# Kernel optimization log

Measured on AMD Instinct MI355X. Metric: run time of the kernel, lower is better.

Reference implementation:

```python
import jax, jax.numpy as jnp
import numpy as np

N_NODES = 20000
N_EDGES = 640000
IN_FEATS = 128
H1, H2 = 64, 32


def setup_inputs() -> dict:
    key = jax.random.key(0)
    ks = jax.random.split(key, 7)
    features = jax.random.normal(ks[0], (N_NODES, IN_FEATS), dtype=jnp.float32)
    W1 = jax.random.normal(ks[1], (IN_FEATS, H1), dtype=jnp.float32) * (1.0 / np.sqrt(IN_FEATS))
    b1 = jax.random.normal(ks[2], (H1,), dtype=jnp.float32) * 0.01
    W2 = jax.random.normal(ks[3], (H1, H2), dtype=jnp.float32) * (1.0 / np.sqrt(H1))
    b2 = jax.random.normal(ks[4], (H2,), dtype=jnp.float32) * 0.01
    src = jax.random.randint(ks[5], (N_EDGES,), 0, N_NODES, dtype=jnp.int32)
    dst = jax.random.randint(ks[6], (N_EDGES,), 0, N_NODES, dtype=jnp.int32)
    return {"features": features, "W1": W1, "b1": b1, "W2": W2, "b2": b2,
            "src": src, "dst": dst}


def _gcn_aggregate(h, src, dst, n_nodes):
    # copy_u + sum: gather source-node features along edges, sum at destinations
    return jax.ops.segment_sum(h[src], dst, num_segments=n_nodes)


def reference(features, W1, b1, W2, b2, src, dst):
    n = features.shape[0]
    # layer 1: aggregate then linear, relu
    h = _gcn_aggregate(features, src, dst, n)          # [N, in_feats]
    x = jax.nn.relu(h @ W1 + b1)                       # [N, 64]
    # layer 2: aggregate then linear
    h2 = _gcn_aggregate(x, src, dst, n)                # [N, 64]
    return h2 @ W2 + b2                                # [N, 32]
```

## Files before the change

kernel.cpp:

```cpp
#include <hip/hip_runtime.h>


#define NF 128
#define H1 64
#define H2 32
#define CAP 128
#define CAPSH 7
#define NG8 8

__device__ __forceinline__ float blo(unsigned u) { return __uint_as_float(u << 16); }
__device__ __forceinline__ float bhi(unsigned u) { return __uint_as_float(u & 0xffff0000u); }
__device__ __forceinline__ unsigned short f2b(float f) {
    unsigned x = __float_as_uint(f);
    return (unsigned short)((x + 0x7fffu + ((x >> 16) & 1u)) >> 16);
}

__global__ void zero_kernel(int* __restrict__ cnt, int n) {
    int i = blockIdx.x * blockDim.x + threadIdx.x;
    if (i < n) cnt[i] = 0;
}

__global__ void fill_kernel(const int* __restrict__ src, const int* __restrict__ dst,
                            int* __restrict__ cnt, unsigned short* __restrict__ slots,
                            int n_edges, int n_nodes) {
    int g = blockIdx.x & (NG8 - 1);
    int gi = blockIdx.x >> 3;
    int sz = (n_nodes + NG8 - 1) / NG8;
    int lo = g * sz;
    unsigned span = (unsigned)(min(lo + sz, n_nodes) - lo);
    int i4 = (gi * blockDim.x + threadIdx.x) * 4;
    if (i4 + 4 <= n_edges) {
        int4 d = *(const int4*)(dst + i4);
        int4 s = *(const int4*)(src + i4);
        int p;
        if ((unsigned)(d.x - lo) < span) { p = atomicAdd(&cnt[d.x], 1); if (p < CAP) slots[(d.x << CAPSH) + p] = (unsigned short)s.x; }
        if ((unsigned)(d.y - lo) < span) { p = atomicAdd(&cnt[d.y], 1); if (p < CAP) slots[(d.y << CAPSH) + p] = (unsigned short)s.y; }
        if ((unsigned)(d.z - lo) < span) { p = atomicAdd(&cnt[d.z], 1); if (p < CAP) slots[(d.z << CAPSH) + p] = (unsigned short)s.z; }
        if ((unsigned)(d.w - lo) < span) { p = atomicAdd(&cnt[d.w], 1); if (p < CAP) slots[(d.w << CAPSH) + p] = (unsigned short)s.w; }
    } else {
        for (int k = i4; k < n_edges; ++k) {
            int d = dst[k];
            if ((unsigned)(d - lo) < span) {
                int p = atomicAdd(&cnt[d], 1);
                if (p < CAP) slots[(d << CAPSH) + p] = (unsigned short)src[k];
            }
        }
    }
}

__launch_bounds__(256)
__global__ void gemm1_kernel(const float* __restrict__ F, const float* __restrict__ W1,
                             unsigned short* __restrict__ P1b, int n_nodes) {
    __shared__ float w[NF][H1];
    const float4* w4 = (const float4*)W1;
    float4* ws4 = (float4*)&w[0][0];
#pragma unroll
    for (int j = 0; j < 8; ++j) ws4[threadIdx.x + 256 * j] = w4[threadIdx.x + 256 * j];
    __syncthreads();
    int wid = threadIdx.x >> 6, lane = threadIdx.x & 63;
#pragma unroll
    for (int r = 0; r < 8; ++r) {
        int row = blockIdx.x * 32 + wid * 8 + r;
        if (row >= n_nodes) break;
        const float4* f4 = (const float4*)(F + (size_t)row * NF);
        float acc = 0.f;
#pragma unroll
        for (int k4 = 0; k4 < NF / 4; ++k4) {
            float4 fv = f4[k4];
            acc += fv.x * w[k4 * 4 + 0][lane];
            acc += fv.y * w[k4 * 4 + 1][lane];
            acc += fv.z * w[k4 * 4 + 2][lane];
            acc += fv.w * w[k4 * 4 + 3][lane];
        }
        P1b[(size_t)row * H1 + lane] = f2b(acc);
    }
}

__launch_bounds__(256)
__global__ void agg1gemm2_kernel(const unsigned short* __restrict__ P1b,
                                 const int* __restrict__ cnt, const unsigned short* __restrict__ slots,
                                 const float* __restrict__ b1, const float* __restrict__ W2,
                                 unsigned short* __restrict__ P2b, int n_nodes) {
    __shared__ float w[H1][H2];
    __shared__ float arow[4][H1];
    const float4* w4 = (const float4*)W2;
    float4* ws4 = (float4*)&w[0][0];
#pragma unroll
    for (int j = 0; j < 2; ++j) ws4[threadIdx.x + 256 * j] = w4[threadIdx.x + 256 * j];
    __syncthreads();
    int wid = threadIdx.x >> 6, lane = threadIdx.x & 63;
    int g = blockIdx.x & (NG8 - 1), gi = blockIdx.x >> 3;
    int sz = (n_nodes + NG8 - 1) / NG8;
    int ni = gi * 4 + wid;
    if (ni >= sz) return;
    int node = g * sz + ni;
    if (node >= n_nodes) return;
    int deg = min(cnt[node], CAP);
    int base = node << CAPSH;
    int half = lane >> 5, c = lane & 31;
    const unsigned* P1u = (const unsigned*)P1b;
    float ax = 0.f, ay = 0.f, bx = 0.f, by = 0.f;
    int i = 0;
    for (; i + 4 <= deg; i += 4) {
        int s0 = slots[base + i + half];
        int s1 = slots[base + i + 2 + half];
        unsigned u0 = P1u[(s0 << 5) + c];
        unsigned u1 = P1u[(s1 << 5) + c];
        ax += blo(u0); ay += bhi(u0);
        bx += blo(u1); by += bhi(u1);
    }
    for (; i + 2 <= deg; i += 2) {
        int s0 = slots[base + i + half];
        unsigned u0 = P1u[(s0 << 5) + c];
        ax += blo(u0); ay += bhi(u0);
    }
    if (i < deg && half == 0) {
        int s0 = slots[base + i];
        unsigned u0 = P1u[(s0 << 5) + c];
        ax += blo(u0); ay += bhi(u0);
    }
    ax += bx; ay += by;
    ax += __shfl_xor(ax, 32, 64);
    ay += __shfl_xor(ay, 32, 64);
    float2 bb = *(const float2*)(b1 + 2 * c);
    float v0 = fmaxf(ax + bb.x, 0.f), v1 = fmaxf(ay + bb.y, 0.f);
    if (lane < 32) *(float2*)&arow[wid][2 * c] = make_float2(v0, v1);
    int kb = half * 32;
    float acc2 = 0.f;
#pragma unroll
    for (int k = 0; k < 32; ++k) acc2 += arow[wid][kb + k] * w[kb + k][c];
    acc2 += __shfl_xor(acc2, 32, 64);
    if (lane < 32) P2b[(size_t)node * H2 + c] = f2b(acc2);
}

__launch_bounds__(256)
__global__ void agg2_kernel(const unsigned short* __restrict__ P2b,
                            const int* __restrict__ cnt, const unsigned short* __restrict__ slots,
                            const float* __restrict__ b2, float* __restrict__ out, int n_nodes) {
    int g = blockIdx.x & (NG8 - 1), gi = blockIdx.x >> 3;
    int sz = (n_nodes + NG8 - 1) / NG8;
    int ni = gi * 8 + (threadIdx.x >> 5);
    if (ni >= sz) return;
    int node = g * sz + ni;
    if (node >= n_nodes) return;
    int l = threadIdx.x & 31;
    int sub = l >> 4, c = l & 15;
    int deg = min(cnt[node], CAP);
    int base = node << CAPSH;
    const unsigned* P2u = (const unsigned*)P2b;
    float ax = 0.f, ay = 0.f, bx = 0.f, by = 0.f;
    int i = 0;
    for (; i + 4 <= deg; i += 4) {
        int s0 = slots[base + i + sub];
        int s1 = slots[base + i + 2 + sub];
        unsigned u0 = P2u[(s0 << 4) + c];
        unsigned u1 = P2u[(s1 << 4) + c];
        ax += blo(u0); ay += bhi(u0);
        bx += blo(u1); by += bhi(u1);
    }
    for (; i + 2 <= deg; i += 2) {
        int s0 = slots[base + i + sub];
        unsigned u0 = P2u[(s0 << 4) + c];
        ax += blo(u0); ay += bhi(u0);
    }
    if (i < deg && sub == 0) {
        int s0 = slots[base + i];
        unsigned u0 = P2u[(s0 << 4) + c];
        ax += blo(u0); ay += bhi(u0);
    }
    ax += bx; ay += by;
    ax += __shfl_xor(ax, 16, 64);
    ay += __shfl_xor(ay, 16, 64);
    if (sub == 0) {
        float2 bb = *(const float2*)(b2 + 2 * c);
        *(float2*)(out + (size_t)node * H2 + 2 * c) = make_float2(ax + bb.x, ay + bb.y);
    }
}

extern "C" void kernel_launch(void* const* d_in, const int* in_sizes, int n_in,
                              void* d_out, int out_size, void* d_ws, size_t ws_size,
                              hipStream_t stream) {
    const float* F  = (const float*)d_in[0];
    const float* W1 = (const float*)d_in[1];
    const float* b1 = (const float*)d_in[2];
    const float* W2 = (const float*)d_in[3];
    const float* b2 = (const float*)d_in[4];
    const int* src  = (const int*)d_in[5];
    const int* dst  = (const int*)d_in[6];
    float* out = (float*)d_out;

    int n_nodes = in_sizes[0] / NF;
    int n_edges = in_sizes[5];

    unsigned short* P1b = (unsigned short*)d_ws;
    unsigned short* P2b = P1b + (size_t)n_nodes * H1;
    unsigned short* slots = P2b + (size_t)n_nodes * H2;
    int* cnt = (int*)(slots + ((size_t)n_nodes << CAPSH));

    int sz = (n_nodes + NG8 - 1) / NG8;

    zero_kernel<<<(n_nodes + 255) / 256, 256, 0, stream>>>(cnt, n_nodes);

    int bpg_fill = ((n_edges + 3) / 4 + 255) / 256;
    fill_kernel<<<bpg_fill * NG8, 256, 0, stream>>>(src, dst, cnt, slots, n_edges, n_nodes);

    gemm1_kernel<<<(n_nodes + 31) / 32, 256, 0, stream>>>(F, W1, P1b, n_nodes);

    int bpg_a1 = (sz + 3) / 4;
    agg1gemm2_kernel<<<bpg_a1 * NG8, 256, 0, stream>>>(P1b, cnt, slots, b1, W2, P2b, n_nodes);

    int bpg_a2 = (sz + 7) / 8;
    agg2_kernel<<<bpg_a2 * NG8, 256, 0, stream>>>(P2b, cnt, slots, b2, out, n_nodes);
}
```

Baseline: 100.2 us.

## Bucket edges by destination group before slot fill and widen aggregation gathers

Replaces the 8x-replicated fill pass, where every block reread all edges and filtered by node group, with a staging kernel. The staging kernel bins packed (dst,src) pairs into per-group buffers using shared-memory counters and one global atomic per group. A second fill kernel then processes only its group's edges. Counter zeroing is folded into the first GEMM kernel, which removes a launch. Both aggregation kernels now gather 8-byte bf16 quads with more edges in flight per wavefront, adding extra shuffle reductions and a staging buffer with a fixed capacity margin.

```diff
diff --git a/kernel.cpp b/kernel.cpp
--- a/kernel.cpp
+++ b/kernel.cpp
@@ -7,6 +7,7 @@
 #define CAP 128
 #define CAPSH 7
 #define NG8 8
+#define FILL_BPG 80
 
 __device__ __forceinline__ float blo(unsigned u) { return __uint_as_float(u << 16); }
 __device__ __forceinline__ float bhi(unsigned u) { return __uint_as_float(u & 0xffff0000u); }
@@ -15,42 +16,12 @@
     return (unsigned short)((x + 0x7fffu + ((x >> 16) & 1u)) >> 16);
 }
 
-__global__ void zero_kernel(int* __restrict__ cnt, int n) {
-    int i = blockIdx.x * blockDim.x + threadIdx.x;
-    if (i < n) cnt[i] = 0;
-}
-
-__global__ void fill_kernel(const int* __restrict__ src, const int* __restrict__ dst,
-                            int* __restrict__ cnt, unsigned short* __restrict__ slots,
-                            int n_edges, int n_nodes) {
-    int g = blockIdx.x & (NG8 - 1);
-    int gi = blockIdx.x >> 3;
-    int sz = (n_nodes + NG8 - 1) / NG8;
-    int lo = g * sz;
-    unsigned span = (unsigned)(min(lo + sz, n_nodes) - lo);
-    int i4 = (gi * blockDim.x + threadIdx.x) * 4;
-    if (i4 + 4 <= n_edges) {
-        int4 d = *(const int4*)(dst + i4);
-        int4 s = *(const int4*)(src + i4);
-        int p;
-        if ((unsigned)(d.x - lo) < span) { p = atomicAdd(&cnt[d.x], 1); if (p < CAP) slots[(d.x << CAPSH) + p] = (unsigned short)s.x; }
-        if ((unsigned)(d.y - lo) < span) { p = atomicAdd(&cnt[d.y], 1); if (p < CAP) slots[(d.y << CAPSH) + p] = (unsigned short)s.y; }
-        if ((unsigned)(d.z - lo) < span) { p = atomicAdd(&cnt[d.z], 1); if (p < CAP) slots[(d.z << CAPSH) + p] = (unsigned short)s.z; }
-        if ((unsigned)(d.w - lo) < span) { p = atomicAdd(&cnt[d.w], 1); if (p < CAP) slots[(d.w << CAPSH) + p] = (unsigned short)s.w; }
-    } else {
-        for (int k = i4; k < n_edges; ++k) {
-            int d = dst[k];
-            if ((unsigned)(d - lo) < span) {
-                int p = atomicAdd(&cnt[d], 1);
-                if (p < CAP) slots[(d << CAPSH) + p] = (unsigned short)src[k];
-            }
-        }
-    }
-}
-
 __launch_bounds__(256)
 __global__ void gemm1_kernel(const float* __restrict__ F, const float* __restrict__ W1,
-                             unsigned short* __restrict__ P1b, int n_nodes) {
+                             unsigned short* __restrict__ P1b, int* __restrict__ cntz,
+                             int n_zero, int n_nodes) {
+    int idx = blockIdx.x * 256 + threadIdx.x;
+    if (idx < n_zero) cntz[idx] = 0;
     __shared__ float w[NF][H1];
     const float4* w4 = (const float4*)W1;
     float4* ws4 = (float4*)&w[0][0];
@@ -77,10 +48,81 @@
 }
 
 __launch_bounds__(256)
+__global__ void stage_kernel(const int* __restrict__ src, const int* __restrict__ dst,
+                             unsigned* __restrict__ staged, int* __restrict__ gcur,
+                             int n_edges, int sz, int capg) {
+    __shared__ int lcnt[NG8];
+    __shared__ int lbase[NG8];
+    int t = threadIdx.x;
+    if (t < NG8) lcnt[t] = 0;
+    __syncthreads();
+    int i4 = (blockIdx.x * 256 + t) * 4;
+    int dd[4], ss[4], bb[4], pp[4];
+    if (i4 + 4 <= n_edges) {
+        int4 d4 = *(const int4*)(dst + i4);
+        int4 s4 = *(const int4*)(src + i4);
+        dd[0] = d4.x; dd[1] = d4.y; dd[2] = d4.z; dd[3] = d4.w;
+        ss[0] = s4.x; ss[1] = s4.y; ss[2] = s4.z; ss[3] = s4.w;
+    } else {
+#pragma unroll
+        for (int k = 0; k < 4; ++k) {
+            int e = i4 + k;
+            dd[k] = (e < n_edges) ? dst[e] : -1;
+            ss[k] = (e < n_edges) ? src[e] : 0;
+        }
+    }
+#pragma unroll
+    for (int k = 0; k < 4; ++k) {
+        if (dd[k] >= 0) {
+            bb[k] = (unsigned)dd[k] / (unsigned)sz;
+            pp[k] = atomicAdd(&lcnt[bb[k]], 1);
+        }
+    }
+    __syncthreads();
+    if (t < NG8) lbase[t] = lcnt[t] ? atomicAdd(&gcur[t], lcnt[t]) : 0;
+    __syncthreads();
+#pragma unroll
+    for (int k = 0; k < 4; ++k) {
+        if (dd[k] >= 0) {
+            int pos = lbase[bb[k]] + pp[k];
+            if (pos < capg)
+                staged[(size_t)bb[k] * capg + pos] = ((unsigned)dd[k] << 16) | (unsigned)ss[k];
+        }
+    }
+}
+
+__launch_bounds__(256)
+__global__ void fill2_kernel(const unsigned* __restrict__ staged, const int* __restrict__ gcur,
+                             int* __restrict__ cnt, unsigned short* __restrict__ slots,
+                             int capg) {
+    int g = blockIdx.x & (NG8 - 1), gi = blockIdx.x >> 3;
+    int ecnt = min(gcur[g], capg);
+    const unsigned* sg = staged + (size_t)g * capg;
+    int stride = FILL_BPG * 256 * 4;
+    for (int j = (gi * 256 + threadIdx.x) * 4; j < ecnt; j += stride) {
+        if (j + 4 <= ecnt) {
+            uint4 u = *(const uint4*)(sg + j);
+            int d, p;
+            d = u.x >> 16; p = atomicAdd(&cnt[d], 1); if (p < CAP) slots[(d << CAPSH) + p] = (unsigned short)(u.x & 0xffffu);
+            d = u.y >> 16; p = atomicAdd(&cnt[d], 1); if (p < CAP) slots[(d << CAPSH) + p] = (unsigned short)(u.y & 0xffffu);
+            d = u.z >> 16; p = atomicAdd(&cnt[d], 1); if (p < CAP) slots[(d << CAPSH) + p] = (unsigned short)(u.z & 0xffffu);
+            d = u.w >> 16; p = atomicAdd(&cnt[d], 1); if (p < CAP) slots[(d << CAPSH) + p] = (unsigned short)(u.w & 0xffffu);
+        } else {
+            for (int k = j; k < ecnt; ++k) {
+                unsigned u = sg[k];
+                int d = u >> 16;
+                int p = atomicAdd(&cnt[d], 1);
+                if (p < CAP) slots[(d << CAPSH) + p] = (unsigned short)(u & 0xffffu);
+            }
+        }
+    }
+}
+
+__launch_bounds__(256)
 __global__ void agg1gemm2_kernel(const unsigned short* __restrict__ P1b,
                                  const int* __restrict__ cnt, const unsigned short* __restrict__ slots,
                                  const float* __restrict__ b1, const float* __restrict__ W2,
-                                 unsigned short* __restrict__ P2b, int n_nodes) {
+                                 unsigned short* __restrict__ P2b, int n_nodes, int sz) {
     __shared__ float w[H1][H2];
     __shared__ float arow[4][H1];
     const float4* w4 = (const float4*)W2;
@@ -90,90 +132,106 @@
     __syncthreads();
     int wid = threadIdx.x >> 6, lane = threadIdx.x & 63;
     int g = blockIdx.x & (NG8 - 1), gi = blockIdx.x >> 3;
-    int sz = (n_nodes + NG8 - 1) / NG8;
     int ni = gi * 4 + wid;
     if (ni >= sz) return;
     int node = g * sz + ni;
     if (node >= n_nodes) return;
     int deg = min(cnt[node], CAP);
     int base = node << CAPSH;
-    int half = lane >> 5, c = lane & 31;
-    const unsigned* P1u = (const unsigned*)P1b;
-    float ax = 0.f, ay = 0.f, bx = 0.f, by = 0.f;
+    int q = lane >> 4, c = lane & 15;
+    const uint2* P1v = (const uint2*)P1b;
+    float a0 = 0.f, a1 = 0.f, a2 = 0.f, a3 = 0.f;
+    float c0 = 0.f, c1 = 0.f, c2 = 0.f, c3 = 0.f;
     int i = 0;
+    for (; i + 8 <= deg; i += 8) {
+        int sA = slots[base + i + q];
+        int sB = slots[base + i + 4 + q];
+        uint2 uA = P1v[(sA << 4) + c];
+        uint2 uB = P1v[(sB << 4) + c];
+        a0 += blo(uA.x); a1 += bhi(uA.x); a2 += blo(uA.y); a3 += bhi(uA.y);
+        c0 += blo(uB.x); c1 += bhi(uB.x); c2 += blo(uB.y); c3 += bhi(uB.y);
+    }
     for (; i + 4 <= deg; i += 4) {
-        int s0 = slots[base + i + half];
-        int s1 = slots[base + i + 2 + half];
-        unsigned u0 = P1u[(s0 << 5) + c];
-        unsigned u1 = P1u[(s1 << 5) + c];
-        ax += blo(u0); ay += bhi(u0);
-        bx += blo(u1); by += bhi(u1);
-    }
-    for (; i + 2 <= deg; i += 2) {
-        int s0 = slots[base + i + half];
-        unsigned u0 = P1u[(s0 << 5) + c];
-        ax += blo(u0); ay += bhi(u0);
-    }
-    if (i < deg && half == 0) {
-        int s0 = slots[base + i];
-        unsigned u0 = P1u[(s0 << 5) + c];
-        ax += blo(u0); ay += bhi(u0);
-    }
-    ax += bx; ay += by;
-    ax += __shfl_xor(ax, 32, 64);
-    ay += __shfl_xor(ay, 32, 64);
-    float2 bb = *(const float2*)(b1 + 2 * c);
-    float v0 = fmaxf(ax + bb.x, 0.f), v1 = fmaxf(ay + bb.y, 0.f);
-    if (lane < 32) *(float2*)&arow[wid][2 * c] = make_float2(v0, v1);
+        int sA = slots[base + i + q];
+        uint2 uA = P1v[(sA << 4) + c];
+        a0 += blo(uA.x); a1 += bhi(uA.x); a2 += blo(uA.y); a3 += bhi(uA.y);
+    }
+    int r = deg - i;
+    if (q < r) {
+        int sA = slots[base + i + q];
+        uint2 uA = P1v[(sA << 4) + c];
+        a0 += blo(uA.x); a1 += bhi(uA.x); a2 += blo(uA.y); a3 += bhi(uA.y);
+    }
+    a0 += c0; a1 += c1; a2 += c2; a3 += c3;
+    a0 += __shfl_xor(a0, 16, 64); a0 += __shfl_xor(a0, 32, 64);
+    a1 += __shfl_xor(a1, 16, 64); a1 += __shfl_xor(a1, 32, 64);
+    a2 += __shfl_xor(a2, 16, 64); a2 += __shfl_xor(a2, 32, 64);
+    a3 += __shfl_xor(a3, 16, 64); a3 += __shfl_xor(a3, 32, 64);
+    if (q == 0) {
+        float4 bb = *(const float4*)(b1 + 4 * c);
+        float4 v;
+        v.x = fmaxf(a0 + bb.x, 0.f);
+        v.y = fmaxf(a1 + bb.y, 0.f);
+        v.z = fmaxf(a2 + bb.z, 0.f);
+        v.w = fmaxf(a3 + bb.w, 0.f);
+        *(float4*)&arow[wid][4 * c] = v;
+    }
+    int half = lane >> 5, c32 = lane & 31;
     int kb = half * 32;
     float acc2 = 0.f;
 #pragma unroll
-    for (int k = 0; k < 32; ++k) acc2 += arow[wid][kb + k] * w[kb + k][c];
+    for (int k = 0; k < 32; ++k) acc2 += arow[wid][kb + k] * w[kb + k][c32];
     acc2 += __shfl_xor(acc2, 32, 64);
-    if (lane < 32) P2b[(size_t)node * H2 + c] = f2b(acc2);
+    if (lane < 32) P2b[(size_t)node * H2 + c32] = f2b(acc2);
 }
 
 __launch_bounds__(256)
 __global__ void agg2_kernel(const unsigned short* __restrict__ P2b,
                             const int* __restrict__ cnt, const unsigned short* __restrict__ slots,
-                            const float* __restrict__ b2, float* __restrict__ out, int n_nodes) {
+                            const float* __restrict__ b2, float* __restrict__ out,
+                            int n_nodes, int sz) {
+    int wid = threadIdx.x >> 6, lane = threadIdx.x & 63;
     int g = blockIdx.x & (NG8 - 1), gi = blockIdx.x >> 3;
-    int sz = (n_nodes + NG8 - 1) / NG8;
-    int ni = gi * 8 + (threadIdx.x >> 5);
+    int ni = gi * 4 + wid;
     if (ni >= sz) return;
     int node = g * sz + ni;
     if (node >= n_nodes) return;
-    int l = threadIdx.x & 31;
-    int sub = l >> 4, c = l & 15;
     int deg = min(cnt[node], CAP);
     int base = node << CAPSH;
-    const unsigned* P2u = (const unsigned*)P2b;
-    float ax = 0.f, ay = 0.f, bx = 0.f, by = 0.f;
+    int o = lane >> 3, c = lane & 7;
+    const uint2* P2v = (const uint2*)P2b;
+    float a0 = 0.f, a1 = 0.f, a2 = 0.f, a3 = 0.f;
+    float c0 = 0.f, c1 = 0.f, c2 = 0.f, c3 = 0.f;
     int i = 0;
-    for (; i + 4 <= deg; i += 4) {
-        int s0 = slots[base + i + sub];
-        int s1 = slots[base + i + 2 + sub];
-        unsigned u0 = P2u[(s0 << 4) + c];
-        unsigned u1 = P2u[(s1 << 4) + c];
-        ax += blo(u0); ay += bhi(u0);
-        bx += blo(u1); by += bhi(u1);
-    }
-    for (; i + 2 <= deg; i += 2) {
-        int s0 = slots[base + i + sub];
-        unsigned u0 = P2u[(s0 << 4) + c];
-        ax += blo(u0); ay += bhi(u0);
-    }
-    if (i < deg && sub == 0) {
-        int s0 = slots[base + i];
-        unsigned u0 = P2u[(s0 << 4) + c];
-        ax += blo(u0); ay += bhi(u0);
-    }
-    ax += bx; ay += by;
-    ax += __shfl_xor(ax, 16, 64);
-    ay += __shfl_xor(ay, 16, 64);
-    if (sub == 0) {
-        float2 bb = *(const float2*)(b2 + 2 * c);
-        *(float2*)(out + (size_t)node * H2 + 2 * c) = make_float2(ax + bb.x, ay + bb.y);
+    for (; i + 16 <= deg; i += 16) {
+        int sA = slots[base + i + o];
+        int sB = slots[base + i + 8 + o];
+        uint2 uA = P2v[(sA << 3) + c];
+        uint2 uB = P2v[(sB << 3) + c];
+        a0 += blo(uA.x); a1 += bhi(uA.x); a2 += blo(uA.y); a3 += bhi(uA.y);
+        c0 += blo(uB.x); c1 += bhi(uB.x); c2 += blo(uB.y); c3 += bhi(uB.y);
+    }
+    for (; i + 8 <= deg; i += 8) {
+        int sA = slots[base + i + o];
+        uint2 uA = P2v[(sA << 3) + c];
+        a0 += blo(uA.x); a1 += bhi(uA.x); a2 += blo(uA.y); a3 += bhi(uA.y);
+    }
+    int r = deg - i;
+    if (o < r) {
+        int sA = slots[base + i + o];
+        uint2 uA = P2v[(sA << 3) + c];
+        a0 += blo(uA.x); a1 += bhi(uA.x); a2 += blo(uA.y); a3 += bhi(uA.y);
+    }
+    a0 += c0; a1 += c1; a2 += c2; a3 += c3;
+    a0 += __shfl_xor(a0, 8, 64); a0 += __shfl_xor(a0, 16, 64); a0 += __shfl_xor(a0, 32, 64);
+    a1 += __shfl_xor(a1, 8, 64); a1 += __shfl_xor(a1, 16, 64); a1 += __shfl_xor(a1, 32, 64);
+    a2 += __shfl_xor(a2, 8, 64); a2 += __shfl_xor(a2, 16, 64); a2 += __shfl_xor(a2, 32, 64);
+    a3 += __shfl_xor(a3, 8, 64); a3 += __shfl_xor(a3, 16, 64); a3 += __shfl_xor(a3, 32, 64);
+    if (o == 0) {
+        float4 bb = *(const float4*)(b2 + 4 * c);
+        float4 v;
+        v.x = a0 + bb.x; v.y = a1 + bb.y; v.z = a2 + bb.z; v.w = a3 + bb.w;
+        *(float4*)(out + (size_t)node * H2 + 4 * c) = v;
     }
 }
 
@@ -191,24 +249,23 @@
 
     int n_nodes = in_sizes[0] / NF;
     int n_edges = in_sizes[5];
+    int sz = (n_nodes + NG8 - 1) / NG8;
+    int capg = n_edges / NG8 + 8192;
 
     unsigned short* P1b = (unsigned short*)d_ws;
     unsigned short* P2b = P1b + (size_t)n_nodes * H1;
     unsigned short* slots = P2b + (size_t)n_nodes * H2;
     int* cnt = (int*)(slots + ((size_t)n_nodes << CAPSH));
-
-    int sz = (n_nodes + NG8 - 1) / NG8;
-
-    zero_kernel<<<(n_nodes + 255) / 256, 256, 0, stream>>>(cnt, n_nodes);
-
-    int bpg_fill = ((n_edges + 3) / 4 + 255) / 256;
-    fill_kernel<<<bpg_fill * NG8, 256, 0, stream>>>(src, dst, cnt, slots, n_edges, n_nodes);
-
-    gemm1_kernel<<<(n_nodes + 31) / 32, 256, 0, stream>>>(F, W1, P1b, n_nodes);
-
-    int bpg_a1 = (sz + 3) / 4;
-    agg1gemm2_kernel<<<bpg_a1 * NG8, 256, 0, stream>>>(P1b, cnt, slots, b1, W2, P2b, n_nodes);
-
-    int bpg_a2 = (sz + 7) / 8;
-    agg2_kernel<<<bpg_a2 * NG8, 256, 0, stream>>>(P2b, cnt, slots, b2, out, n_nodes);
-}
+    int* gcur = cnt + n_nodes;
+    unsigned* staged = (unsigned*)(gcur + NG8);
+
+    gemm1_kernel<<<(n_nodes + 31) / 32, 256, 0, stream>>>(F, W1, P1b, cnt,
+                                                          n_nodes + NG8, n_nodes);
+    stage_kernel<<<(n_edges + 1023) / 1024, 256, 0, stream>>>(src, dst, staged, gcur,
+                                                              n_edges, sz, capg);
+    fill2_kernel<<<FILL_BPG * NG8, 256, 0, stream>>>(staged, gcur, cnt, slots, capg);
+
+    int bpg = (sz + 3) / 4;
+    agg1gemm2_kernel<<<bpg * NG8, 256, 0, stream>>>(P1b, cnt, slots, b1, W2, P2b, n_nodes, sz);
+    agg2_kernel<<<bpg * NG8, 256, 0, stream>>>(P2b, cnt, slots, b2, out, n_nodes, sz);
+}
```

Result: faster. 97.30 us (-2.9%).
